# Performance work log

Hardware: AMD Instinct MI355X
Metric: run time of the kernel (lower is better)

Reference implementation:

```python
import jax, jax.numpy as jnp
import numpy as np

B, H, W, DIN = 512, 14, 14, 512
EDIM, K = 64, 256
GRID = 2  # code grid -> code_seq_len = 4


def setup_inputs() -> dict:
    key = jax.random.key(0)
    ks = jax.random.split(key, 12)
    def lin(k, fin, fout):
        return jax.random.normal(k, (fin, fout), jnp.float32) / np.sqrt(fin).astype(np.float32)
    return {
        "features_t0": jax.random.normal(ks[0], (B, H, W, DIN), jnp.float32),
        "features_t1": jax.random.normal(ks[1], (B, H, W, DIN), jnp.float32),
        "enc_w1": lin(ks[2], DIN, 2 * EDIM), "enc_b1": jnp.zeros((2 * EDIM,), jnp.float32),
        "enc_w2": lin(ks[3], 2 * EDIM, EDIM), "enc_b2": jnp.zeros((EDIM,), jnp.float32),
        "dec_w1": lin(ks[4], EDIM, 2 * EDIM), "dec_b1": jnp.zeros((2 * EDIM,), jnp.float32),
        "dec_w2": lin(ks[5], 2 * EDIM, DIN), "dec_b2": jnp.zeros((DIN,), jnp.float32),
        "codebook": jax.random.normal(ks[6], (K, EDIM), jnp.float32),
    }


def reference(features_t0, features_t1, enc_w1, enc_b1, enc_w2, enc_b2,
              dec_w1, dec_b1, dec_w2, dec_b2, codebook):
    # eval-mode forward (no EMA update / data init)
    delta = features_t1 - features_t0                       # [B,H,W,DIN]
    h = jax.nn.gelu(delta @ enc_w1 + enc_b1, approximate=False)
    e = h @ enc_w2 + enc_b2                                 # [B,H,W,EDIM]
    # AdaptiveAvgPool2d((2,2)) on 14x14 == exact 7x7 block mean
    bh, bw = H // GRID, W // GRID
    pooled = e.reshape(B, GRID, bh, GRID, bw, EDIM).mean(axis=(2, 4))  # [B,2,2,EDIM]
    enc = pooled.reshape(B, GRID * GRID, EDIM)              # [B,4,EDIM]

    flat = enc.reshape(-1, EDIM)                            # [B*4, EDIM]
    d2 = ((flat ** 2).sum(-1, keepdims=True)
          - 2.0 * flat @ codebook.T
          + (codebook ** 2).sum(-1))                        # [N,K]
    idx = jnp.argmin(d2, axis=1)                            # [N]
    quantized = codebook[idx]                               # [N,EDIM]

    commitment_loss = jnp.mean((jax.lax.stop_gradient(quantized) - flat) ** 2)
    q_st = flat + jax.lax.stop_gradient(quantized - flat)   # straight-through

    n_tok = flat.shape[0]
    avg_probs = jnp.zeros((K,), flat.dtype).at[idx].add(1.0) / n_tok
    perplexity = jnp.exp(-jnp.sum(avg_probs * jnp.log(avg_probs + 1e-10)))

    q = q_st.reshape(B, GRID * GRID, EDIM)
    hd = jax.nn.gelu(q @ dec_w1 + dec_b1, approximate=False)
    dec = hd @ dec_w2 + dec_b2                              # [B,4,DIN]
    sp = dec.reshape(B, GRID, GRID, DIN).transpose(0, 3, 1, 2)  # [B,DIN,2,2]
    # bilinear, align_corners=False (half-pixel centers, matches jax.image.resize)
    up = jax.image.resize(sp, (B, DIN, H, W), method="bilinear")
    decoded = up.transpose(0, 2, 3, 1)                      # [B,H,W,DIN]

    indices = idx.reshape(B, GRID * GRID)
    return decoded, perplexity, commitment_loss, indices
```

## Files before the change

### kernel.cpp

```cpp
#include <hip/hip_runtime.h>
#include <math.h>

#define N_TOKENS   2048
#define DECODED_SZ 51380224

__device__ __forceinline__ float gelu_exact(float x) {
    return 0.5f * x * (1.0f + erff(x * 0.70710678118654752440f));
}

__global__ __launch_bounds__(512, 4) void k1_enc_pool(
    const float* __restrict__ t0, const float* __restrict__ t1,
    const float* __restrict__ w1, const float* __restrict__ b1,
    float* __restrict__ pooled)
{
    __shared__ float sW[32 * 128];
    __shared__ float sD[196 * 36];

    const int t  = threadIdx.x;
    const int b  = blockIdx.x;
    const int ng = t & 15;
    const int g  = t >> 4;
    const int tk = g >> 3;
    const int sub = g & 7;
    const int ty = tk >> 1, tx = tk & 1;

    const float4* __restrict__ w1v = reinterpret_cast<const float4*>(w1);
    const float4* __restrict__ t0v = reinterpret_cast<const float4*>(t0);
    const float4* __restrict__ t1v = reinterpret_cast<const float4*>(t1);

    const float* rowp[7];
#pragma unroll
    for (int mm = 0; mm < 7; ++mm) {
        int r = sub * 7 + mm;
        if (r > 48) r = 48;
        int m = (ty * 7 + r / 7) * 14 + tx * 7 + (r % 7);
        rowp[mm] = sD + m * 36;
    }

    float acc[7][8] = {};

    for (int kc = 0; kc < 16; ++kc) {
#pragma unroll
        for (int i = 0; i < 2; ++i) {
            int idx4 = t + i * 512;
            reinterpret_cast<float4*>(sW)[idx4] = w1v[kc * 1024 + idx4];
        }
        for (int i = t; i < 1568; i += 512) {
            int m = i >> 3, j = i & 7;
            int g4 = (b * 196 + m) * 128 + kc * 8 + j;
            float4 a = t1v[g4];
            float4 c = t0v[g4];
            float4 d;
            d.x = a.x - c.x; d.y = a.y - c.y; d.z = a.z - c.z; d.w = a.w - c.w;
            reinterpret_cast<float4*>(sD + m * 36)[j] = d;
        }
        __syncthreads();

        for (int kk = 0; kk < 32; kk += 2) {
            const float* wr0 = sW + kk * 128;
            const float* wr1 = wr0 + 128;
            const float4 wa0 = *reinterpret_cast<const float4*>(wr0 + 4 * ng);
            const float4 wb0 = *reinterpret_cast<const float4*>(wr0 + 64 + 4 * ng);
            const float4 wa1 = *reinterpret_cast<const float4*>(wr1 + 4 * ng);
            const float4 wb1 = *reinterpret_cast<const float4*>(wr1 + 64 + 4 * ng);
#pragma unroll
            for (int mm = 0; mm < 7; ++mm) {
                const float2 dv = *reinterpret_cast<const float2*>(rowp[mm] + kk);
                float* A = acc[mm];
                A[0] = fmaf(dv.x, wa0.x, A[0]);
                A[1] = fmaf(dv.x, wa0.y, A[1]);
                A[2] = fmaf(dv.x, wa0.z, A[2]);
                A[3] = fmaf(dv.x, wa0.w, A[3]);
                A[4] = fmaf(dv.x, wb0.x, A[4]);
                A[5] = fmaf(dv.x, wb0.y, A[5]);
                A[6] = fmaf(dv.x, wb0.z, A[6]);
                A[7] = fmaf(dv.x, wb0.w, A[7]);
                A[0] = fmaf(dv.y, wa1.x, A[0]);
                A[1] = fmaf(dv.y, wa1.y, A[1]);
                A[2] = fmaf(dv.y, wa1.z, A[2]);
                A[3] = fmaf(dv.y, wa1.w, A[3]);
                A[4] = fmaf(dv.y, wb1.x, A[4]);
                A[5] = fmaf(dv.y, wb1.y, A[5]);
                A[6] = fmaf(dv.y, wb1.z, A[6]);
                A[7] = fmaf(dv.y, wb1.w, A[7]);
            }
        }
        __syncthreads();
    }

    const float4 ba = *reinterpret_cast<const float4*>(b1 + 4 * ng);
    const float4 bb = *reinterpret_cast<const float4*>(b1 + 64 + 4 * ng);
    float p[8] = {};
#pragma unroll
    for (int mm = 0; mm < 7; ++mm) {
        int r = sub * 7 + mm;
        if (r < 49) {
            p[0] += gelu_exact(acc[mm][0] + ba.x);
            p[1] += gelu_exact(acc[mm][1] + ba.y);
            p[2] += gelu_exact(acc[mm][2] + ba.z);
            p[3] += gelu_exact(acc[mm][3] + ba.w);
            p[4] += gelu_exact(acc[mm][4] + bb.x);
            p[5] += gelu_exact(acc[mm][5] + bb.y);
            p[6] += gelu_exact(acc[mm][6] + bb.z);
            p[7] += gelu_exact(acc[mm][7] + bb.w);
        }
    }
    float* sR = sW;
    {
        float4 pa; pa.x = p[0]; pa.y = p[1]; pa.z = p[2]; pa.w = p[3];
        float4 pb; pb.x = p[4]; pb.y = p[5]; pb.z = p[6]; pb.w = p[7];
        *reinterpret_cast<float4*>(sR + g * 128 + 4 * ng)      = pa;
        *reinterpret_cast<float4*>(sR + g * 128 + 64 + 4 * ng) = pb;
    }
    __syncthreads();
    {
        const int tk2 = t >> 7;
        const int ch  = t & 127;
        float s = 0.f;
#pragma unroll
        for (int ss = 0; ss < 8; ++ss) s += sR[(tk2 * 8 + ss) * 128 + ch];
        pooled[(b * 4 + tk2) * 128 + ch] = s * (1.0f / 49.0f);
    }
}

__global__ __launch_bounds__(256, 2) void k2_mid(
    const float* __restrict__ pooled,
    const float* __restrict__ w2,  const float* __restrict__ b2,
    const float* __restrict__ cb,
    const float* __restrict__ dw1, const float* __restrict__ db1,
    const float* __restrict__ dw2, const float* __restrict__ db2,
    float* __restrict__ dec, float* __restrict__ hist, float* __restrict__ commit,
    float* __restrict__ out_idx)
{
    __shared__ float sCB[256 * 66];
    __shared__ float ph[4 * 128];
    __shared__ float es[4 * 64];
    __shared__ float hd[4 * 128];
    __shared__ float rd[256];
    __shared__ int   ri[256];
    __shared__ int   idxs[4];
    __shared__ float dms[4];

    const int t   = threadIdx.x;
    const int tk0 = blockIdx.x * 4;

    if (t < 128)
        reinterpret_cast<float4*>(ph)[t] =
            reinterpret_cast<const float4*>(pooled + tk0 * 128)[t];
    for (int i = t; i < 16384; i += 256) {
        int row = i >> 6, k = i & 63;
        sCB[row * 66 + k] = cb[i];
    }
    __syncthreads();

    {
        const int j = t & 63, tok = t >> 6;
        float a = b2[j];
        const float* phr = ph + tok * 128;
#pragma unroll 8
        for (int k = 0; k < 128; ++k)
            a = fmaf(phr[k], w2[k * 64 + j], a);
        es[tok * 64 + j] = a;
    }
    __syncthreads();

    {
        const int tok = t >> 6, c8 = t & 63;
        float2 ev[32];
#pragma unroll
        for (int k = 0; k < 32; ++k)
            ev[k] = *reinterpret_cast<const float2*>(es + tok * 64 + 2 * k);
        float dmin = 3.4e38f; int imin = 0;
#pragma unroll
        for (int cc = 0; cc < 4; ++cc) {
            const int c = c8 + cc * 64;
            const float* cr = sCB + c * 66;
            float d = 0.f;
#pragma unroll
            for (int k = 0; k < 32; ++k) {
                float2 c2 = *reinterpret_cast<const float2*>(cr + 2 * k);
                float d0 = ev[k].x - c2.x;
                float d1 = ev[k].y - c2.y;
                d = fmaf(d0, d0, d);
                d = fmaf(d1, d1, d);
            }
            if (d < dmin || (d == dmin && c < imin)) { dmin = d; imin = c; }
        }
        rd[t] = dmin; ri[t] = imin;
    }
    __syncthreads();
    for (int s = 32; s > 0; s >>= 1) {
        if ((t & 63) < s) {
            float dn = rd[t + s]; int in = ri[t + s];
            if (dn < rd[t] || (dn == rd[t] && in < ri[t])) { rd[t] = dn; ri[t] = in; }
        }
        __syncthreads();
    }
    if ((t & 63) == 0) {
        const int tok = t >> 6;
        idxs[tok] = ri[t];
        dms[tok]  = rd[t];
        out_idx[tk0 + tok] = (float)ri[t];
        atomicAdd(&hist[ri[t]], 1.0f);
    }
    __syncthreads();
    if (t == 0) {
        float s = dms[0] + dms[1] + dms[2] + dms[3];
        atomicAdd(commit, s);
    }

    {
        const int j = t & 127, half = t >> 7;
        const float bj = db1[j];
        float a0 = bj, a1 = bj;
        const float* q0 = sCB + idxs[half * 2 + 0] * 66;
        const float* q1 = sCB + idxs[half * 2 + 1] * 66;
#pragma unroll 4
        for (int k = 0; k < 64; ++k) {
            const float wv = dw1[k * 128 + j];
            a0 = fmaf(q0[k], wv, a0);
            a1 = fmaf(q1[k], wv, a1);
        }
        hd[(half * 2 + 0) * 128 + j] = gelu_exact(a0);
        hd[(half * 2 + 1) * 128 + j] = gelu_exact(a1);
    }
    __syncthreads();

    {
        float a0[4], a1[4];
        const float bb0 = db2[t], bb1 = db2[t + 256];
#pragma unroll
        for (int q = 0; q < 4; ++q) { a0[q] = bb0; a1[q] = bb1; }
#pragma unroll 2
        for (int j = 0; j < 128; ++j) {
            const float w0 = dw2[j * 512 + t];
            const float w1v = dw2[j * 512 + 256 + t];
#pragma unroll
            for (int q = 0; q < 4; ++q) {
                const float h = hd[q * 128 + j];
                a0[q] = fmaf(h, w0, a0[q]);
                a1[q] = fmaf(h, w1v, a1[q]);
            }
        }
#pragma unroll
        for (int q = 0; q < 4; ++q) {
            dec[(tk0 + q) * 512 + t]       = a0[q];
            dec[(tk0 + q) * 512 + 256 + t] = a1[q];
        }
    }
}

__global__ __launch_bounds__(256) void k2b_final(
    const float* __restrict__ hist, const float* __restrict__ commit,
    float* __restrict__ out2)
{
    __shared__ float red[256];
    const int t = threadIdx.x;
    float p = hist[t] * (1.0f / 2048.0f);
    red[t] = p * logf(p + 1e-10f);
    __syncthreads();
    for (int s = 128; s > 0; s >>= 1) {
        if (t < s) red[t] += red[t + s];
        __syncthreads();
    }
    if (t == 0) {
        out2[0] = expf(-red[0]);
        out2[1] = commit[0] * (1.0f / 131072.0f);
    }
}

__global__ __launch_bounds__(256, 4) void k3_upsample(
    const float* __restrict__ dec, float* __restrict__ out)
{
    __shared__ float  sdec[4 * 512];
    __shared__ float4 wts[196];
    __shared__ int4   offs[196];
    const int b = blockIdx.x, t = threadIdx.x;

    for (int i = t; i < 512; i += 256)
        reinterpret_cast<float4*>(sdec)[i] =
            reinterpret_cast<const float4*>(dec + b * 2048)[i];
    if (t < 196) {
        const int y = t / 14, x = t % 14;
        const float sy = (y + 0.5f) * (1.0f / 7.0f) - 0.5f;
        const float sx = (x + 0.5f) * (1.0f / 7.0f) - 0.5f;
        const int iy = (int)floorf(sy), ix = (int)floorf(sx);
        const float fy = sy - (float)iy, fx = sx - (float)ix;
        const int y0 = min(max(iy, 0), 1), y1 = min(max(iy + 1, 0), 1);
        const int x0 = min(max(ix, 0), 1), x1 = min(max(ix + 1, 0), 1);
        float4 w;
        w.x = (1.f - fy) * (1.f - fx); w.y = (1.f - fy) * fx;
        w.z = fy * (1.f - fx);         w.w = fy * fx;
        wts[t] = w;
        int4 o;
        o.x = (y0 * 2 + x0) * 128; o.y = (y0 * 2 + x1) * 128;
        o.z = (y1 * 2 + x0) * 128; o.w = (y1 * 2 + x1) * 128;
        offs[t] = o;
    }
    __syncthreads();

    const float4* s4 = reinterpret_cast<const float4*>(sdec);
    float4* o4 = reinterpret_cast<float4*>(out) + b * 25088;
    const int c4 = t & 127, ph2 = t >> 7;

#pragma unroll 2
    for (int it = 0; it < 98; ++it) {
        const int pos = ph2 + it * 2;
        const float4 w = wts[pos];
        const int4   o = offs[pos];
        const float4 v00 = s4[o.x + c4];
        const float4 v01 = s4[o.y + c4];
        const float4 v10 = s4[o.z + c4];
        const float4 v11 = s4[o.w + c4];
        float4 r;
        r.x = w.x * v00.x + w.y * v01.x + w.z * v10.x + w.w * v11.x;
        r.y = w.x * v00.y + w.y * v01.y + w.z * v10.y + w.w * v11.y;
        r.z = w.x * v00.z + w.y * v01.z + w.z * v10.z + w.w * v11.z;
        r.w = w.x * v00.w + w.y * v01.w + w.z * v10.w + w.w * v11.w;
        o4[pos * 128 + c4] = r;
    }
}

extern "C" void kernel_launch(void* const* d_in, const int* in_sizes, int n_in,
                              void* d_out, int out_size, void* d_ws, size_t ws_size,
                              hipStream_t stream)
{
    const float* t0  = (const float*)d_in[0];
    const float* t1  = (const float*)d_in[1];
    const float* w1  = (const float*)d_in[2];
    const float* b1  = (const float*)d_in[3];
    const float* w2  = (const float*)d_in[4];
    const float* b2  = (const float*)d_in[5];
    const float* dw1 = (const float*)d_in[6];
    const float* db1 = (const float*)d_in[7];
    const float* dw2 = (const float*)d_in[8];
    const float* db2 = (const float*)d_in[9];
    const float* cb  = (const float*)d_in[10];

    float* out = (float*)d_out;
    float* ws  = (float*)d_ws;

    float* pooled = ws;
    float* dec    = ws + 262144;
    float* hist   = ws + 1310720;
    float* commit = ws + 1310976;

    hipMemsetAsync(hist, 0, 257 * sizeof(float), stream);

    k1_enc_pool<<<512, 512, 0, stream>>>(t0, t1, w1, b1, pooled);
    k2_mid<<<512, 256, 0, stream>>>(pooled, w2, b2, cb, dw1, db1, dw2, db2,
                                    dec, hist, commit, out + DECODED_SZ + 2);
    k2b_final<<<1, 256, 0, stream>>>(hist, commit, out + DECODED_SZ);
    k3_upsample<<<512, 256, 0, stream>>>(dec, out);
}
```

Before: 652.1 us.

## Use split-bf16 MFMA for the encoder first-layer GEMM with fused pooling

Replaces the scalar FP32 FMA GEMM in the encoder first layer with bf16 MFMA 32x32x16 instructions. FP32 accuracy is approximated by splitting both operands into high and low bf16 parts and summing three products. A new prep kernel converts and transposes w1 into bf16 hi/lo tiles in workspace that aliases the dec buffer, which is written later. The GELU and 7x7 pooling epilogue is remapped to the MFMA output layout with cross-lane shuffles. This targets the compute-bound encoder GEMM, at the cost of three times the MFMA work, extra conversion ALU in the load path, and slightly lower precision.

After: 648.6 us. Within noise of the previous version (-0.5%).

```diff
diff --git a/kernel.cpp b/kernel.cpp
--- a/kernel.cpp
+++ b/kernel.cpp
@@ -4,122 +4,167 @@
 #define N_TOKENS   2048
 #define DECODED_SZ 51380224
 
+typedef __attribute__((ext_vector_type(8)))  short bf16x8;
+typedef __attribute__((ext_vector_type(16))) float f32x16;
+
 __device__ __forceinline__ float gelu_exact(float x) {
     return 0.5f * x * (1.0f + erff(x * 0.70710678118654752440f));
 }
 
-__global__ __launch_bounds__(512, 4) void k1_enc_pool(
+__device__ __forceinline__ unsigned int f2bf(float x) {
+    unsigned int u = __float_as_uint(x);
+    return (u + 0x7fffu + ((u >> 16) & 1u)) >> 16;
+}
+__device__ __forceinline__ float bf2f(unsigned int b) {
+    return __uint_as_float(b << 16);
+}
+
+__global__ __launch_bounds__(256) void k0_prep_w1(
+    const float* __restrict__ w1,
+    unsigned short* __restrict__ bth, unsigned short* __restrict__ btl)
+{
+    const int i  = blockIdx.x * 256 + threadIdx.x;
+    const int n  = i >> 6;
+    const int kg = i & 63;
+    const int k0i = kg * 8;
+
+    unsigned int h[8], lo[8];
+#pragma unroll
+    for (int j = 0; j < 8; ++j) {
+        float v = w1[(k0i + j) * 128 + n];
+        h[j]  = f2bf(v);
+        lo[j] = f2bf(v - bf2f(h[j]));
+    }
+    const int idx = (k0i >> 5) * 4096 + n * 32 + (k0i & 31);
+    uint4 hv, lv;
+    hv.x = h[0]  | (h[1] << 16);  hv.y = h[2]  | (h[3] << 16);
+    hv.z = h[4]  | (h[5] << 16);  hv.w = h[6]  | (h[7] << 16);
+    lv.x = lo[0] | (lo[1] << 16); lv.y = lo[2] | (lo[3] << 16);
+    lv.z = lo[4] | (lo[5] << 16); lv.w = lo[6] | (lo[7] << 16);
+    *reinterpret_cast<uint4*>(bth + idx) = hv;
+    *reinterpret_cast<uint4*>(btl + idx) = lv;
+}
+
+__global__ __launch_bounds__(256, 2) void k1_enc_pool(
     const float* __restrict__ t0, const float* __restrict__ t1,
-    const float* __restrict__ w1, const float* __restrict__ b1,
+    const unsigned short* __restrict__ bth, const unsigned short* __restrict__ btl,
+    const float* __restrict__ b1,
     float* __restrict__ pooled)
 {
-    __shared__ float sW[32 * 128];
-    __shared__ float sD[196 * 36];
-
-    const int t  = threadIdx.x;
-    const int b  = blockIdx.x;
-    const int ng = t & 15;
-    const int g  = t >> 4;
-    const int tk = g >> 3;
-    const int sub = g & 7;
-    const int ty = tk >> 1, tx = tk & 1;
-
-    const float4* __restrict__ w1v = reinterpret_cast<const float4*>(w1);
+    __shared__ unsigned short sAh[256 * 40];
+    __shared__ unsigned short sAl[256 * 40];
+    __shared__ unsigned short sBh[128 * 40];
+    __shared__ unsigned short sBl[128 * 40];
+    __shared__ float sR[2 * 4 * 128];
+
+    const int t = threadIdx.x;
+    const int b = blockIdx.x;
+    const int l     = t & 63;
+    const int w     = t >> 6;
+    const int wm    = w >> 1;
+    const int wn    = w & 1;
+    const int lan31 = l & 31;
+    const int h     = l >> 5;
+
     const float4* __restrict__ t0v = reinterpret_cast<const float4*>(t0);
     const float4* __restrict__ t1v = reinterpret_cast<const float4*>(t1);
 
-    const float* rowp[7];
-#pragma unroll
-    for (int mm = 0; mm < 7; ++mm) {
-        int r = sub * 7 + mm;
-        if (r > 48) r = 48;
-        int m = (ty * 7 + r / 7) * 14 + tx * 7 + (r % 7);
-        rowp[mm] = sD + m * 36;
-    }
-
-    float acc[7][8] = {};
+    f32x16 acc[4][2] = {};
 
     for (int kc = 0; kc < 16; ++kc) {
-#pragma unroll
-        for (int i = 0; i < 2; ++i) {
-            int idx4 = t + i * 512;
-            reinterpret_cast<float4*>(sW)[idx4] = w1v[kc * 1024 + idx4];
-        }
-        for (int i = t; i < 1568; i += 512) {
-            int m = i >> 3, j = i & 7;
-            int g4 = (b * 196 + m) * 128 + kc * 8 + j;
-            float4 a = t1v[g4];
-            float4 c = t0v[g4];
-            float4 d;
-            d.x = a.x - c.x; d.y = a.y - c.y; d.z = a.z - c.z; d.w = a.w - c.w;
-            reinterpret_cast<float4*>(sD + m * 36)[j] = d;
-        }
         __syncthreads();
-
-        for (int kk = 0; kk < 32; kk += 2) {
-            const float* wr0 = sW + kk * 128;
-            const float* wr1 = wr0 + 128;
-            const float4 wa0 = *reinterpret_cast<const float4*>(wr0 + 4 * ng);
-            const float4 wb0 = *reinterpret_cast<const float4*>(wr0 + 64 + 4 * ng);
-            const float4 wa1 = *reinterpret_cast<const float4*>(wr1 + 4 * ng);
-            const float4 wb1 = *reinterpret_cast<const float4*>(wr1 + 64 + 4 * ng);
-#pragma unroll
-            for (int mm = 0; mm < 7; ++mm) {
-                const float2 dv = *reinterpret_cast<const float2*>(rowp[mm] + kk);
-                float* A = acc[mm];
-                A[0] = fmaf(dv.x, wa0.x, A[0]);
-                A[1] = fmaf(dv.x, wa0.y, A[1]);
-                A[2] = fmaf(dv.x, wa0.z, A[2]);
-                A[3] = fmaf(dv.x, wa0.w, A[3]);
-                A[4] = fmaf(dv.x, wb0.x, A[4]);
-                A[5] = fmaf(dv.x, wb0.y, A[5]);
-                A[6] = fmaf(dv.x, wb0.z, A[6]);
-                A[7] = fmaf(dv.x, wb0.w, A[7]);
-                A[0] = fmaf(dv.y, wa1.x, A[0]);
-                A[1] = fmaf(dv.y, wa1.y, A[1]);
-                A[2] = fmaf(dv.y, wa1.z, A[2]);
-                A[3] = fmaf(dv.y, wa1.w, A[3]);
-                A[4] = fmaf(dv.y, wb1.x, A[4]);
-                A[5] = fmaf(dv.y, wb1.y, A[5]);
-                A[6] = fmaf(dv.y, wb1.z, A[6]);
-                A[7] = fmaf(dv.y, wb1.w, A[7]);
-            }
+        for (int i = t; i < 196 * 8; i += 256) {
+            const int m = i >> 3, j = i & 7;
+            const int g4 = (b * 196 + m) * 128 + kc * 8 + j;
+            const float4 a = t1v[g4];
+            const float4 c = t0v[g4];
+            const float dx = a.x - c.x, dy = a.y - c.y, dz = a.z - c.z, dw = a.w - c.w;
+            const unsigned int h0 = f2bf(dx), h1 = f2bf(dy), h2 = f2bf(dz), h3 = f2bf(dw);
+            const unsigned int l0 = f2bf(dx - bf2f(h0)), l1 = f2bf(dy - bf2f(h1));
+            const unsigned int l2 = f2bf(dz - bf2f(h2)), l3 = f2bf(dw - bf2f(h3));
+            uint2 hv, lv;
+            hv.x = h0 | (h1 << 16); hv.y = h2 | (h3 << 16);
+            lv.x = l0 | (l1 << 16); lv.y = l2 | (l3 << 16);
+            *reinterpret_cast<uint2*>(&sAh[m * 40 + j * 4]) = hv;
+            *reinterpret_cast<uint2*>(&sAl[m * 40 + j * 4]) = lv;
+        }
+        for (int i = t; i < 1024; i += 256) {
+            const int sel = i >> 9;
+            const int i2 = i & 511;
+            const int col = i2 >> 2, j8 = i2 & 3;
+            const uint4 v = *reinterpret_cast<const uint4*>(
+                (sel ? btl : bth) + kc * 4096 + col * 32 + j8 * 8);
+            *reinterpret_cast<uint4*>(&(sel ? sBl : sBh)[col * 40 + j8 * 8]) = v;
         }
         __syncthreads();
-    }
-
-    const float4 ba = *reinterpret_cast<const float4*>(b1 + 4 * ng);
-    const float4 bb = *reinterpret_cast<const float4*>(b1 + 64 + 4 * ng);
-    float p[8] = {};
-#pragma unroll
-    for (int mm = 0; mm < 7; ++mm) {
-        int r = sub * 7 + mm;
-        if (r < 49) {
-            p[0] += gelu_exact(acc[mm][0] + ba.x);
-            p[1] += gelu_exact(acc[mm][1] + ba.y);
-            p[2] += gelu_exact(acc[mm][2] + ba.z);
-            p[3] += gelu_exact(acc[mm][3] + ba.w);
-            p[4] += gelu_exact(acc[mm][4] + bb.x);
-            p[5] += gelu_exact(acc[mm][5] + bb.y);
-            p[6] += gelu_exact(acc[mm][6] + bb.z);
-            p[7] += gelu_exact(acc[mm][7] + bb.w);
-        }
-    }
-    float* sR = sW;
-    {
-        float4 pa; pa.x = p[0]; pa.y = p[1]; pa.z = p[2]; pa.w = p[3];
-        float4 pb; pb.x = p[4]; pb.y = p[5]; pb.z = p[6]; pb.w = p[7];
-        *reinterpret_cast<float4*>(sR + g * 128 + 4 * ng)      = pa;
-        *reinterpret_cast<float4*>(sR + g * 128 + 64 + 4 * ng) = pb;
-    }
-    __syncthreads();
-    {
-        const int tk2 = t >> 7;
-        const int ch  = t & 127;
-        float s = 0.f;
-#pragma unroll
-        for (int ss = 0; ss < 8; ++ss) s += sR[(tk2 * 8 + ss) * 128 + ch];
-        pooled[(b * 4 + tk2) * 128 + ch] = s * (1.0f / 49.0f);
+
+#pragma unroll
+        for (int ks = 0; ks < 2; ++ks) {
+            const int koff = ks * 16 + h * 8;
+            bf16x8 ah[4], al[4], bhf[2], blf[2];
+#pragma unroll
+            for (int mi = 0; mi < 4; ++mi) {
+                const int row = (wm * 4 + mi) * 32 + lan31;
+                ah[mi] = *reinterpret_cast<const bf16x8*>(&sAh[row * 40 + koff]);
+                al[mi] = *reinterpret_cast<const bf16x8*>(&sAl[row * 40 + koff]);
+            }
+#pragma unroll
+            for (int ni = 0; ni < 2; ++ni) {
+                const int col = (wn * 2 + ni) * 32 + lan31;
+                bhf[ni] = *reinterpret_cast<const bf16x8*>(&sBh[col * 40 + koff]);
+                blf[ni] = *reinterpret_cast<const bf16x8*>(&sBl[col * 40 + koff]);
+            }
+#pragma unroll
+            for (int mi = 0; mi < 4; ++mi) {
+#pragma unroll
+                for (int ni = 0; ni < 2; ++ni) {
+                    acc[mi][ni] = __builtin_amdgcn_mfma_f32_32x32x16_bf16(
+                        ah[mi], bhf[ni], acc[mi][ni], 0, 0, 0);
+                    acc[mi][ni] = __builtin_amdgcn_mfma_f32_32x32x16_bf16(
+                        ah[mi], blf[ni], acc[mi][ni], 0, 0, 0);
+                    acc[mi][ni] = __builtin_amdgcn_mfma_f32_32x32x16_bf16(
+                        al[mi], bhf[ni], acc[mi][ni], 0, 0, 0);
+                }
+            }
+        }
+    }
+
+    float tokacc[2][4] = {};
+#pragma unroll
+    for (int ni = 0; ni < 2; ++ni) {
+        const int col = (wn * 2 + ni) * 32 + lan31;
+        const float bias = b1[col];
+#pragma unroll
+        for (int mi = 0; mi < 4; ++mi) {
+#pragma unroll
+            for (int reg = 0; reg < 16; ++reg) {
+                const int row = (wm * 4 + mi) * 32 + (reg & 3) + 8 * (reg >> 2) + 4 * h;
+                if (row < 196) {
+                    const float v = gelu_exact(acc[mi][ni][reg] + bias);
+                    const int py = row / 14, px = row % 14;
+                    const int tok = ((py >= 7) ? 2 : 0) + ((px >= 7) ? 1 : 0);
+                    tokacc[ni][tok] += v;
+                }
+            }
+        }
+    }
+#pragma unroll
+    for (int ni = 0; ni < 2; ++ni)
+#pragma unroll
+        for (int tok = 0; tok < 4; ++tok)
+            tokacc[ni][tok] += __shfl_xor(tokacc[ni][tok], 32);
+    if (h == 0) {
+#pragma unroll
+        for (int ni = 0; ni < 2; ++ni)
+#pragma unroll
+            for (int tok = 0; tok < 4; ++tok)
+                sR[(wm * 4 + tok) * 128 + wn * 64 + ni * 32 + lan31] = tokacc[ni][tok];
+    }
+    __syncthreads();
+    for (int i = t; i < 512; i += 256) {
+        const int tok = i >> 7, col = i & 127;
+        pooled[(b * 4 + tok) * 128 + col] =
+            (sR[tok * 128 + col] + sR[(4 + tok) * 128 + col]) * (1.0f / 49.0f);
     }
 }
 
@@ -345,9 +390,13 @@
     float* hist   = ws + 1310720;
     float* commit = ws + 1310976;
 
+    unsigned short* bth = (unsigned short*)(ws + 262144);
+    unsigned short* btl = (unsigned short*)(ws + 262144 + 32768);
+
     hipMemsetAsync(hist, 0, 257 * sizeof(float), stream);
 
-    k1_enc_pool<<<512, 512, 0, stream>>>(t0, t1, w1, b1, pooled);
+    k0_prep_w1<<<32, 256, 0, stream>>>(w1, bth, btl);
+    k1_enc_pool<<<512, 256, 0, stream>>>(t0, t1, bth, btl, b1, pooled);
     k2_mid<<<512, 256, 0, stream>>>(pooled, w2, b2, cb, dw1, db1, dw2, db2,
                                     dec, hist, commit, out + DECODED_SZ + 2);
     k2b_final<<<1, 256, 0, stream>>>(hist, commit, out + DECODED_SZ);
```
